# Performance work log

Hardware: AMD Instinct MI355X
Metric: run time of the kernel (lower is better)

The kernel has to match this reference:

```python
import jax, jax.numpy as jnp
import numpy as np

# pywt db3 analysis filters (dec_lo, dec_hi)
DB3_LO = np.array([0.035226291882100656, -0.08544127388224149, -0.13501102001039084,
                   0.4598775021193313, 0.8068915093133388, 0.3326705529509569], dtype=np.float32)
DB3_HI = np.array([-0.3326705529509569, 0.8068915093133388, -0.4598775021193313,
                   -0.13501102001039084, 0.08544127388224149, 0.035226291882100656], dtype=np.float32)
L_FILT = 6
J_LEVELS = 3
EPS = 1e-8


def _dwt_level(x):
    """One analysis level, zero-padding ('zero' mode, matches pywt/pytorch_wavelets).
    x: [B, N] -> (low [B, M], high [B, M]) with M = floor((N + L - 1) / 2).
    Uses true convolution (filters flipped) of the full zero-extended signal,
    downsampled at odd full-conv indices, implemented as one strided conv."""
    k = jnp.asarray(np.stack([DB3_LO[::-1], DB3_HI[::-1]])[:, None, :])  # [2,1,L]
    y = jax.lax.conv_general_dilated(x[:, None, :].astype(jnp.float32), k,
                                     window_strides=(2,),
                                     padding=[(L_FILT - 2, L_FILT - 1)])  # [B,2,M]
    return y[:, 0, :], y[:, 1, :]


def _dwt_stats(signals):
    """signals: [B, N]. Returns (mean of final low band, sum over levels of L2 norm
    of each high band) per row -- exactly what the torch loop computes per entity."""
    x = signals
    high_energy = jnp.zeros(signals.shape[0], signals.dtype)
    for _ in range(J_LEVELS):
        lo, hi = _dwt_level(x)
        high_energy = high_energy + jnp.sqrt(jnp.sum(hi * hi, axis=-1))
        x = lo
    return jnp.mean(x, axis=-1), high_energy


def _dirichlet_weight(key, low, high):
    a1 = jnp.clip(low, 1e-6)
    a2 = jnp.clip(high, 1e-6)
    s = a1 + a2
    a1, a2 = a1 / s, a2 / s
    # first component of Dirichlet([10*a1, 10*a2]) ~ Beta(10*a1, 10*a2)
    return jax.random.beta(key, 10.0 * a1, 10.0 * a2)


def setup_inputs() -> dict:
    key = jax.random.key(0)
    k1, k2, k3 = jax.random.split(key, 3)
    U, I, NNZ = 16384, 8192, 1000000
    user_idx = jax.random.randint(k1, (NNZ,), 0, U, dtype=jnp.int32)
    item_idx = jax.random.randint(k2, (NNZ,), 0, I, dtype=jnp.int32)
    values = jax.random.uniform(k3, (NNZ,), dtype=jnp.float32)
    return {"user_idx": user_idx, "item_idx": item_idx, "values": values,
            "num_users": U, "num_items": I}


def reference(user_idx, item_idx, values, num_users, num_items):
    # item popularity
    counts = jax.ops.segment_sum(jnp.ones_like(values), item_idx, num_segments=num_items)
    log_counts = jnp.log1p(counts)
    pop = jax.ops.segment_sum(values * log_counts[item_idx], item_idx, num_segments=num_items)
    pop = pop / (jnp.linalg.norm(pop) + EPS)
    # user activity
    act = jax.ops.segment_sum(values / jnp.log1p(pop[item_idx] + EPS),
                              user_idx, num_segments=num_users)
    act = act / (jnp.linalg.norm(act) + EPS)
    # batched dense signals + DWT (replaces per-entity python loop)
    Su = jnp.zeros((num_users, num_items), values.dtype).at[user_idx, item_idx].set(
        values * (1.0 + act[user_idx]))
    u_low, u_high = _dwt_stats(Su)
    Si = jnp.zeros((num_items, num_users), values.dtype).at[item_idx, user_idx].set(
        values * (1.0 + pop[item_idx]))
    i_low, i_high = _dwt_stats(Si)
    ku, ki = jax.random.split(jax.random.key(42))
    upw = _dirichlet_weight(ku, u_low, u_high)
    ipw = _dirichlet_weight(ki, i_low, i_high)
    return (upw, 1.0 - upw, ipw, 1.0 - ipw, act, pop)
```

## Files before the change

kernel.cpp:

```cpp
#include <hip/hip_runtime.h>
#include <stdint.h>

#define PARTITIONABLE 1

typedef unsigned long long ull;

#define NUM_U 16384
#define NUM_I 8192
#define CAP_U 160
#define CAP_I 256

#define OFF_UPW 0
#define OFF_UMW 16384
#define OFF_IPW 32768
#define OFF_IMW 40960
#define OFF_ACT 49152
#define OFF_POP 65536

struct K2 { uint32_t a, b; };

__host__ __device__ inline void tf2x32(uint32_t k0, uint32_t k1, uint32_t& x0, uint32_t& x1) {
  const uint32_t ks2 = k0 ^ k1 ^ 0x1BD11BDAu;
  x0 += k0; x1 += k1;
#define TF_R(r) { x0 += x1; x1 = (x1 << (r)) | (x1 >> (32 - (r))); x1 ^= x0; }
  TF_R(13) TF_R(15) TF_R(26) TF_R(6)
  x0 += k1; x1 += ks2 + 1u;
  TF_R(17) TF_R(29) TF_R(16) TF_R(24)
  x0 += ks2; x1 += k0 + 2u;
  TF_R(13) TF_R(15) TF_R(26) TF_R(6)
  x0 += k0; x1 += k1 + 3u;
  TF_R(17) TF_R(29) TF_R(16) TF_R(24)
  x0 += k1; x1 += ks2 + 4u;
  TF_R(13) TF_R(15) TF_R(26) TF_R(6)
  x0 += ks2; x1 += k0 + 5u;
#undef TF_R
}

__host__ __device__ inline K2 tf_enc(K2 k, uint32_t x0, uint32_t x1) {
  tf2x32(k.a, k.b, x0, x1);
  K2 r; r.a = x0; r.b = x1; return r;
}

__host__ __device__ inline void split2(K2 k, K2& c0, K2& c1) {
#if PARTITIONABLE
  c0 = tf_enc(k, 0u, 0u);
  c1 = tf_enc(k, 0u, 1u);
#else
  K2 p = tf_enc(k, 0u, 2u);
  K2 q = tf_enc(k, 1u, 3u);
  c0.a = p.a; c0.b = q.a;
  c1.a = p.b; c1.b = q.b;
#endif
}

__device__ inline void split3(K2 k, K2& c0, K2& c1, K2& c2) {
#if PARTITIONABLE
  c0 = tf_enc(k, 0u, 0u);
  c1 = tf_enc(k, 0u, 1u);
  c2 = tf_enc(k, 0u, 2u);
#else
  K2 p = tf_enc(k, 0u, 3u);
  K2 q = tf_enc(k, 1u, 4u);
  K2 r = tf_enc(k, 2u, 5u);
  c0.a = p.a; c0.b = q.a;
  c1.a = r.a; c1.b = p.b;
  c2.a = q.b; c2.b = r.b;
#endif
}

__device__ inline uint32_t draw_bits(K2 k) {
  K2 e = tf_enc(k, 0u, 0u);
#if PARTITIONABLE
  return e.a ^ e.b;
#else
  return e.a;
#endif
}

__device__ inline K2 elem_key(K2 k, uint32_t i, uint32_t B) {
#if PARTITIONABLE
  return tf_enc(k, 0u, i);
#else
  if (i < (B >> 1)) {
    K2 p = tf_enc(k, 2u * i, B + 2u * i);
    K2 q = tf_enc(k, 2u * i + 1u, B + 2u * i + 1u);
    K2 r; r.a = p.a; r.b = q.a; return r;
  } else {
    uint32_t j = 2u * i - B;
    K2 p = tf_enc(k, j, 2u * i);
    K2 q = tf_enc(k, j + 1u, 2u * i + 1u);
    K2 r; r.a = p.b; r.b = q.b; return r;
  }
#endif
}

__device__ inline float u01_bits(uint32_t b) {
  return __uint_as_float((b >> 9) | 0x3F800000u) - 1.0f;
}

__device__ inline float erfinv_f32(float x) {
  float w = -log1pf(-x * x);
  float p;
  if (w < 5.0f) {
    w = w - 2.5f;
    p = 2.81022636e-08f;
    p = fmaf(p, w, 3.43273939e-07f);
    p = fmaf(p, w, -3.5233877e-06f);
    p = fmaf(p, w, -4.39150654e-06f);
    p = fmaf(p, w, 0.00021858087f);
    p = fmaf(p, w, -0.00125372503f);
    p = fmaf(p, w, -0.00417768164f);
    p = fmaf(p, w, 0.246640727f);
    p = fmaf(p, w, 1.50140941f);
  } else {
    w = sqrtf(w) - 3.0f;
    p = -0.000200214257f;
    p = fmaf(p, w, 0.000100950558f);
    p = fmaf(p, w, 0.00134934322f);
    p = fmaf(p, w, -0.00367342844f);
    p = fmaf(p, w, 0.00573950773f);
    p = fmaf(p, w, -0.0076224613f);
    p = fmaf(p, w, 0.00943887047f);
    p = fmaf(p, w, 1.00167406f);
    p = fmaf(p, w, 2.83297682f);
  }
  return p * x;
}

__device__ float log_gamma_sample(K2 key, float alpha_orig) {
  const bool boost = (alpha_orig >= 1.0f);
  const float alpha = boost ? alpha_orig : (alpha_orig + 1.0f);
  const float d = alpha - 0.33333334f;
  const float c = 0.33333334f / sqrtf(d);

  K2 k0, sub;
  split2(key, k0, sub);
  const float u_boost = u01_bits(draw_bits(sub));

  K2 kcur = k0;
  float X = 0.0f, V = 1.0f, U = 2.0f;
  while ((U >= 1.0f - 0.0331f * (X * X)) &&
         (logf(U) >= X * 0.5f + d * ((1.0f - V) + logf(V)))) {
    K2 knext, xk, Uk;
    split3(kcur, knext, xk, Uk);
    kcur = knext;
    float x, v;
    K2 ik = xk;
    do {
      K2 in0, isub;
      split2(ik, in0, isub);
      ik = in0;
      float f = u01_bits(draw_bits(isub));
      float u = fmaxf(-0.99999994f, f * 2.0f + (-0.99999994f));
      x = 1.41421356f * erfinv_f32(u);
      v = 1.0f + x * c;
    } while (v <= 0.0f);
    X = x * x;
    V = (v * v) * v;
    U = u01_bits(draw_bits(Uk));
  }
  float lg = logf(d * V);
  if (!boost) lg += log1pf(-u_boost) / alpha_orig;
  return lg;
}


__global__ __launch_bounds__(256) void zero_kernel(ull* p, int n) {
  int i = blockIdx.x * 256 + threadIdx.x;
  if (i < n) p[i] = 0ull;
}

__global__ __launch_bounds__(256) void count_fill_kernel(
    const int* __restrict__ user, const int* __restrict__ item, int n,
    int* __restrict__ fu, int* __restrict__ fi,
    uint32_t* __restrict__ lu, uint32_t* __restrict__ li) {
  for (int k = blockIdx.x * 256 + threadIdx.x; k < n; k += gridDim.x * 256) {
    int it = item[k];
    int q = atomicAdd(&fi[it], 1);
    if (q < CAP_I) li[(size_t)it * CAP_I + q] = (uint32_t)k;
    int u = user[k];
    int p = atomicAdd(&fu[u], 1);
    if (p < CAP_U) lu[(size_t)u * CAP_U + p] = (uint32_t)k;
  }
}

__global__ __launch_bounds__(256) void pop_wave_kernel(
    const int* __restrict__ fi, const uint32_t* __restrict__ li,
    const float* __restrict__ values,
    float* __restrict__ pop, double* __restrict__ nrm2) {
  __shared__ float red[4];
  int lane = threadIdx.x & 63, wid = threadIdx.x >> 6;
  int i = blockIdx.x * 4 + wid;
  int cnt = fi[i];
  int cr = cnt < CAP_I ? cnt : CAP_I;
  long long s = 0;
  for (int e = lane; e < cr; e += 64)
    s += (long long)llrintf(values[li[(size_t)i * CAP_I + e]] * 4294967296.0f);
  for (int o = 32; o > 0; o >>= 1) s += __shfl_down(s, o);
  if (lane == 0) {
    float svf = (float)((double)(ull)s * (1.0 / 4294967296.0));
    float p = svf * log1pf((float)cnt);
    pop[i] = p;
    red[wid] = p * p;
  }
  __syncthreads();
  if (threadIdx.x == 0)
    atomicAdd(nrm2, (double)(red[0] + red[1] + red[2] + red[3]));
}

__global__ __launch_bounds__(256) void pop_norm_kernel(float* __restrict__ pop,
                                                       const double* __restrict__ nrm2,
                                                       float* __restrict__ out) {
  int i = blockIdx.x * 256 + threadIdx.x;
  if (i < NUM_I) {
    float nrm = sqrtf((float)(*nrm2));
    float v = pop[i] / (nrm + 1e-8f);
    pop[i] = v;
    out[OFF_POP + i] = v;
  }
}

__global__ __launch_bounds__(256) void act_wave_kernel(
    const int* __restrict__ fu, const uint32_t* __restrict__ lu,
    const int* __restrict__ item, const float* __restrict__ values,
    const float* __restrict__ pop,
    float* __restrict__ act, double* __restrict__ nrm2) {
  __shared__ float red[4];
  int lane = threadIdx.x & 63, wid = threadIdx.x >> 6;
  int u = blockIdx.x * 4 + wid;
  int cnt = fu[u];
  int cr = cnt < CAP_U ? cnt : CAP_U;
  long long s = 0;
  for (int e = lane; e < cr; e += 64) {
    uint32_t k = lu[(size_t)u * CAP_U + e];
    float term = values[k] / log1pf(pop[item[k]] + 1e-8f);
    s += (long long)llrintf(term * 16777216.0f);
  }
  for (int o = 32; o > 0; o >>= 1) s += __shfl_down(s, o);
  if (lane == 0) {
    float a = (float)((double)(ull)s * (1.0 / 16777216.0));
    act[u] = a;
    red[wid] = a * a;
  }
  __syncthreads();
  if (threadIdx.x == 0)
    atomicAdd(nrm2, (double)(red[0] + red[1] + red[2] + red[3]));
}

__global__ __launch_bounds__(256) void act_norm_kernel(float* __restrict__ act,
                                                       const double* __restrict__ nrm2,
                                                       float* __restrict__ out) {
  int u = blockIdx.x * 256 + threadIdx.x;
  if (u < NUM_U) {
    float nrm = sqrtf((float)(*nrm2));
    float v = act[u] / (nrm + 1e-8f);
    act[u] = v;
    out[OFF_ACT + u] = v;
  }
}

__device__ inline uint32_t evencomp(uint32_t x) {
  x = (x | (x >> 1)) & 0x55555555u;
  x = (x | (x >> 1)) & 0x33333333u;
  x = (x | (x >> 2)) & 0x0F0F0F0Fu;
  x = (x | (x >> 4)) & 0x00FF00FFu;
  x = (x | (x >> 8)) & 0x0000FFFFu;
  return x;
}
template <int NWIN>
__device__ inline uint32_t hword(const uint32_t* B, int i) {
  uint32_t a = (2 * i < NWIN) ? B[2 * i] : 0u;
  uint32_t b = (2 * i + 1 < NWIN) ? B[2 * i + 1] : 0u;
  return evencomp(a) | (evencomp(b) << 16);
}
template <int NWIN>
__device__ inline uint32_t tword(const uint32_t* B, int w) {
  uint32_t h = hword<NWIN>(B, w);
  uint32_t hp = (w > 0) ? hword<NWIN>(B, w - 1) : 0u;
  return h | (h << 1) | (h << 2) | (hp >> 31) | (hp >> 30);
}

template <int NWORDS>
__device__ inline int scan_bits(const uint32_t* __restrict__ W, uint16_t* __restrict__ P,
                                int tid, int* __restrict__ isc, int* __restrict__ tot) {
  constexpr int WPT = (NWORDS + 255) / 256;
  __syncthreads();
  uint32_t w[WPT];
  int v = 0;
#pragma unroll
  for (int j = 0; j < WPT; ++j) {
    int idx = tid * WPT + j;
    w[j] = (idx < NWORDS) ? W[idx] : 0u;
    v += __popc(w[j]);
  }
  int lane = tid & 63, wid = tid >> 6;
  int incl = v;
  for (int off = 1; off < 64; off <<= 1) {
    int y = __shfl_up(incl, off, 64);
    if (lane >= off) incl += y;
  }
  if (lane == 63) isc[wid] = incl;
  __syncthreads();
  int base = 0;
  for (int ww = 0; ww < wid; ++ww) base += isc[ww];
  int run = base + incl - v;
#pragma unroll
  for (int j = 0; j < WPT; ++j) {
    int idx = tid * WPT + j;
    if (idx < NWORDS) P[idx] = (uint16_t)run;
    run += __popc(w[j]);
  }
  if (tid == 255) *tot = run;
  __syncthreads();
  return *tot;
}

template <int NWORDS>
__device__ inline void build_wl(const uint32_t* __restrict__ T, const uint16_t* __restrict__ P,
                                uint16_t* __restrict__ wl, int tid) {
  for (int w = tid; w < NWORDS; w += 256) {
    uint32_t bits = T[w];
    int r0 = P[w], i = 0;
    while (bits) {
      int b = __ffs(bits) - 1; bits &= bits - 1u;
      wl[r0 + i] = (uint16_t)((w << 5) + b);
      ++i;
    }
  }
}

template <int NIN>
__device__ inline void gather6(const uint32_t* __restrict__ B, const uint16_t* __restrict__ P,
                               const float* __restrict__ V, int m,
                               float& lo_o, float& hi_o) {
  int c0 = 2 * m - 4; c0 = c0 < 0 ? 0 : c0;
  int c1 = 2 * m + 1; c1 = c1 > NIN - 1 ? NIN - 1 : c1;
  int w0 = c0 >> 5, w1 = c1 >> 5;
  uint32_t b0 = B[w0];
  uint32_t mlo = ~((1u << (c0 & 31)) - 1u);
  uint32_t mhi = (uint32_t)(((uint64_t)1u << ((c1 & 31) + 1)) - 1u);
  uint32_t sel0, sel1; uint32_t b1 = 0;
  if (w1 == w0) { sel0 = b0 & mlo & mhi; sel1 = 0u; }
  else { b1 = B[w1]; sel0 = b0 & mlo; sel1 = b1 & mhi; }
  float tv0 = 0.0f, tv1 = 0.0f, tv2 = 0.0f, tv3 = 0.0f, tv4 = 0.0f, tv5 = 0.0f;
  int tp1 = 2 * m + 1;
  uint32_t s = sel0;
  while (s) {
    int b = __ffs(s) - 1; s &= s - 1u;
    int c = (w0 << 5) + b;
    int idx = (int)P[w0] + __popc(b0 & ((1u << b) - 1u));
    float v = V[idx];
    int t = tp1 - c;
    if (t == 0) tv0 = v; else if (t == 1) tv1 = v; else if (t == 2) tv2 = v;
    else if (t == 3) tv3 = v; else if (t == 4) tv4 = v; else tv5 = v;
  }
  s = sel1;
  while (s) {
    int b = __ffs(s) - 1; s &= s - 1u;
    int c = (w1 << 5) + b;
    int idx = (int)P[w1] + __popc(b1 & ((1u << b) - 1u));
    float v = V[idx];
    int t = tp1 - c;
    if (t == 0) tv0 = v; else if (t == 1) tv1 = v; else if (t == 2) tv2 = v;
    else if (t == 3) tv3 = v; else if (t == 4) tv4 = v; else tv5 = v;
  }
  float lo = 0.0f, hi = 0.0f;
  lo += 0.035226291882100656f * tv0;  hi += -0.3326705529509569f * tv0;
  lo += -0.08544127388224149f * tv1;  hi += 0.8068915093133388f * tv1;
  lo += -0.13501102001039084f * tv2;  hi += -0.4598775021193313f * tv2;
  lo += 0.4598775021193313f * tv3;    hi += -0.13501102001039084f * tv3;
  lo += 0.8068915093133388f * tv4;    hi += 0.08544127388224149f * tv4;
  lo += 0.3326705529509569f * tv5;    hi += 0.035226291882100656f * tv5;
  lo_o = lo; hi_o = hi;
}

__device__ inline int rank_of(const uint32_t* __restrict__ B, const uint16_t* __restrict__ P,
                              int m) {
  int w = m >> 5;
  return (int)P[w] + __popc(B[w] & ((1u << (m & 31)) - 1u));
}

constexpr int align4c(int x) { return (x + 3) & ~3; }
constexpr int cmax(int a, int b) { return a > b ? a : b; }

constexpr int dwt_shm_bytes(int NCOLS, int M1, int M2, int M3, int CAP) {
  int NW = NCOLS / 32, NW1 = (M1 + 31) / 32, NW2 = (M2 + 31) / 32, NW3 = (M3 + 31) / 32;
  int SZ_RB = cmax(cmax(align4c(NW * 4 + NW * 2), align4c(NW2 * 4 + 4 * CAP * 2)),
                   align4c(5 * CAP * 2));
  int SZ_RC = cmax(align4c(NW1 * 4 + NW1 * 2), align4c(NW3 * 4 + NW3 * 2 + NW2 * 2));
  return (M1 + 12) * 4 + CAP * 4 + SZ_RB + SZ_RC + align4c(3 * CAP * 2) + 64;
}

template <int NCOLS, int M1, int M2, int M3, int CAP>
__global__ __launch_bounds__(256) void dwt_rows_kernel(
    const uint32_t* __restrict__ klist, const int* __restrict__ rowlen,
    const int* __restrict__ colsrc, const float* __restrict__ values,
    const float* __restrict__ scale_vec,
    float* __restrict__ low_out, float* __restrict__ high_out) {
  constexpr int NW = NCOLS / 32;
  constexpr int NW1 = (M1 + 31) / 32;
  constexpr int NW2 = (M2 + 31) / 32;
  constexpr int NW3 = (M3 + 31) / 32;
  constexpr uint32_t MK1 = (M1 & 31) ? ((1u << (M1 & 31)) - 1u) : 0xFFFFFFFFu;
  constexpr uint32_t MK2 = (M2 & 31) ? ((1u << (M2 & 31)) - 1u) : 0xFFFFFFFFu;
  constexpr uint32_t MK3 = (M3 & 31) ? ((1u << (M3 & 31)) - 1u) : 0xFFFFFFFFu;
  constexpr int SZ_RB = cmax(cmax(align4c(NW * 4 + NW * 2), align4c(NW2 * 4 + 4 * CAP * 2)),
                             align4c(5 * CAP * 2));
  constexpr int SZ_RC = cmax(align4c(NW1 * 4 + NW1 * 2), align4c(NW3 * 4 + NW3 * 2 + NW2 * 2));

  extern __shared__ char smroot[];
  float* buf = (float*)smroot;
  char* pA = smroot + (M1 + 12) * 4;
  int* slot = (int*)pA;
  float* sval = (float*)pA;
  char* pB = pA + CAP * 4;
  uint32_t* bitmap = (uint32_t*)pB;
  uint16_t* prefix = (uint16_t*)(pB + NW * 4);
  uint32_t* T2 = (uint32_t*)pB;
  uint16_t* wl2 = (uint16_t*)(pB + NW2 * 4);
  uint16_t* wl3 = (uint16_t*)pB;
  char* pC = pB + SZ_RB;
  uint32_t* T1 = (uint32_t*)pC;
  uint16_t* p1 = (uint16_t*)(pC + NW1 * 4);
  uint32_t* T3 = (uint32_t*)pC;
  uint16_t* p3 = (uint16_t*)(pC + NW3 * 4);
  uint16_t* p2 = (uint16_t*)(pC + NW3 * 4 + NW3 * 2);
  char* pD = pC + SZ_RC;
  uint16_t* wl1 = (uint16_t*)pD;
  char* pE = pD + align4c(3 * CAP * 2);
  int* isc = (int*)pE;
  int* tot = isc + 4;
  float* red = (float*)pE;

  const int r = blockIdx.x;
  const int tid = threadIdx.x;
  const float scale = 1.0f + scale_vec[r];
  int n = rowlen[r];
  if (n > CAP) n = CAP;
  const size_t krow = (size_t)r * CAP;

  {
    constexpr int NB4 = (M1 + 12) / 4;
    float4 z; z.x = 0.0f; z.y = 0.0f; z.z = 0.0f; z.w = 0.0f;
    for (int i = tid; i < NB4; i += 256) ((float4*)buf)[i] = z;
    for (int i = NB4 * 4 + tid; i < M1 + 12; i += 256) buf[i] = 0.0f;
  }
  for (int i = tid; i < NW; i += 256) bitmap[i] = 0u;
  for (int i = tid; i < CAP; i += 256) slot[i] = 0;
  __syncthreads();

  for (int e = tid; e < n; e += 256) {
    int c = colsrc[klist[krow + e]];
    atomicOr(&bitmap[c >> 5], 1u << (c & 31));
  }
  const int nw_cnt = scan_bits<NW>(bitmap, prefix, tid, isc, tot);

  for (int e = tid; e < n; e += 256) {
    uint32_t k = klist[krow + e];
    int c = colsrc[k];
    atomicMax(&slot[rank_of(bitmap, prefix, c)], (int)k + 1);
  }
  __syncthreads();

  for (int rr = tid; rr < nw_cnt; rr += 256)
    sval[rr] = values[slot[rr] - 1] * scale;
  for (int w = tid; w < NW1; w += 256) {
    uint32_t t = tword<NW>(bitmap, w);
    if (w == NW1 - 1) t &= MK1;
    T1[w] = t;
  }
  const int n1 = scan_bits<NW1>(T1, p1, tid, isc, tot);
  build_wl<NW1>(T1, p1, wl1, tid);
  __syncthreads();

  float h1 = 0.0f;
  for (int idx = tid; idx < n1; idx += 256) {
    int m = wl1[idx];
    float lo, hi;
    gather6<NCOLS>(bitmap, prefix, sval, m, lo, hi);
    buf[4 + m] = lo;
    h1 += hi * hi;
  }
  __syncthreads();

  for (int w = tid; w < NW2; w += 256) {
    uint32_t t = tword<NW1>(T1, w);
    if (w == NW2 - 1) t &= MK2;
    T2[w] = t;
  }
  const int n2 = scan_bits<NW2>(T2, p2, tid, isc, tot);
  build_wl<NW2>(T2, p2, wl2, tid);
  for (int w = tid; w < NW3; w += 256) {
    uint32_t t = tword<NW2>(T2, w);
    if (w == NW3 - 1) t &= MK3;
    T3[w] = t;
  }
  __syncthreads();

  float h2 = 0.0f;
  {
    int nb = (n2 + 255) >> 8;
    for (int b = 0; b < nb; ++b) {
      int idx = (b << 8) + tid;
      bool ok = idx < n2;
      int m = ok ? wl2[idx] : 0;
      const float* s = buf + 2 * m + 5;
      float x0 = s[0], x1 = s[-1], x2 = s[-2], x3 = s[-3], x4 = s[-4], x5 = s[-5];
      __syncthreads();
      if (ok) {
        float lo = 0.0f, hi = 0.0f;
        lo += 0.035226291882100656f * x0;  hi += -0.3326705529509569f * x0;
        lo += -0.08544127388224149f * x1;  hi += 0.8068915093133388f * x1;
        lo += -0.13501102001039084f * x2;  hi += -0.4598775021193313f * x2;
        lo += 0.4598775021193313f * x3;    hi += -0.13501102001039084f * x3;
        lo += 0.8068915093133388f * x4;    hi += 0.08544127388224149f * x4;
        lo += 0.3326705529509569f * x5;    hi += 0.035226291882100656f * x5;
        buf[4 + m] = lo;
        h2 += hi * hi;
      }
    }
  }
  __syncthreads();
  for (int idx = tid; idx < n1; idx += 256) {
    int m = wl1[idx];
    if (m < M2 && !((T2[m >> 5] >> (m & 31)) & 1u)) buf[4 + m] = 0.0f;
  }
  if (tid < 8) buf[4 + M2 + tid] = 0.0f;

  const int n3 = scan_bits<NW3>(T3, p3, tid, isc, tot);
  build_wl<NW3>(T3, p3, wl3, tid);
  __syncthreads();

  float h3 = 0.0f, slo = 0.0f;
  for (int idx = tid; idx < n3; idx += 256) {
    int m = wl3[idx];
    const float* s = buf + 2 * m + 5;
    float x0 = s[0], x1 = s[-1], x2 = s[-2], x3 = s[-3], x4 = s[-4], x5 = s[-5];
    float lo = 0.0f, hi = 0.0f;
    lo += 0.035226291882100656f * x0;  hi += -0.3326705529509569f * x0;
    lo += -0.08544127388224149f * x1;  hi += 0.8068915093133388f * x1;
    lo += -0.13501102001039084f * x2;  hi += -0.4598775021193313f * x2;
    lo += 0.4598775021193313f * x3;    hi += -0.13501102001039084f * x3;
    lo += 0.8068915093133388f * x4;    hi += 0.08544127388224149f * x4;
    lo += 0.3326705529509569f * x5;    hi += 0.035226291882100656f * x5;
    slo += lo;
    h3 += hi * hi;
  }

  for (int o = 32; o > 0; o >>= 1) {
    h1 += __shfl_down(h1, o);
    h2 += __shfl_down(h2, o);
    h3 += __shfl_down(h3, o);
    slo += __shfl_down(slo, o);
  }
  __syncthreads();
  int w = tid >> 6, lane = tid & 63;
  if (lane == 0) { red[w] = h1; red[4 + w] = h2; red[8 + w] = h3; red[12 + w] = slo; }
  __syncthreads();
  if (tid == 0) {
    float s1 = red[0] + red[1] + red[2] + red[3];
    float s2 = red[4] + red[5] + red[6] + red[7];
    float s3 = red[8] + red[9] + red[10] + red[11];
    float sl = red[12] + red[13] + red[14] + red[15];
    low_out[r] = sl / (float)M3;
    high_out[r] = sqrtf(s1) + sqrtf(s2) + sqrtf(s3);
  }
}

__global__ __launch_bounds__(256) void beta_kernel(
    const float* __restrict__ u_low, const float* __restrict__ u_high,
    const float* __restrict__ i_low, const float* __restrict__ i_high,
    float* __restrict__ out, K2 kAu, K2 kBu, K2 kAi, K2 kBi) {
  int t = blockIdx.x * 256 + threadIdx.x;
  if (t >= NUM_U + NUM_I) return;
  float low, high;
  K2 ka, kb;
  int o0, o1;
  if (t < NUM_U) {
    low = u_low[t]; high = u_high[t];
    ka = elem_key(kAu, (uint32_t)t, (uint32_t)NUM_U);
    kb = elem_key(kBu, (uint32_t)t, (uint32_t)NUM_U);
    o0 = OFF_UPW + t; o1 = OFF_UMW + t;
  } else {
    int j = t - NUM_U;
    low = i_low[j]; high = i_high[j];
    ka = elem_key(kAi, (uint32_t)j, (uint32_t)NUM_I);
    kb = elem_key(kBi, (uint32_t)j, (uint32_t)NUM_I);
    o0 = OFF_IPW + j; o1 = OFF_IMW + j;
  }
  float a1 = fmaxf(low, 1e-6f);
  float a2 = fmaxf(high, 1e-6f);
  float s = a1 + a2;
  a1 = a1 / s;
  a2 = a2 / s;
  float lga = log_gamma_sample(ka, 10.0f * a1);
  float lgb = log_gamma_sample(kb, 10.0f * a2);
  float m = fmaxf(lga, lgb);
  float na = expf(lga - m);
  float nb = expf(lgb - m);
  float w = na / (na + nb);
  out[o0] = w;
  out[o1] = 1.0f - w;
}

extern "C" void kernel_launch(void* const* d_in, const int* in_sizes, int n_in,
                              void* d_out, int out_size, void* d_ws, size_t ws_size,
                              hipStream_t stream) {
  const int* user_idx = (const int*)d_in[0];
  const int* item_idx = (const int*)d_in[1];
  const float* values = (const float*)d_in[2];
  const int NNZ = in_sizes[0];

  char* ws = (char*)d_ws;
  double* nrm2_pop = (double*)(ws + 0);
  double* nrm2_act = (double*)(ws + 8);
  float* pop = (float*)(ws + 229392);
  float* act = (float*)(ws + 262160);
  int* fill_u = (int*)(ws + 327696);
  int* fill_i = (int*)(ws + 393232);
  float* u_low = (float*)(ws + 426000);
  float* u_high = (float*)(ws + 491536);
  float* i_low = (float*)(ws + 557072);
  float* i_high = (float*)(ws + 589840);
  uint32_t* klist_u = (uint32_t*)(ws + 622608);
  uint32_t* klist_i = (uint32_t*)(ws + 11108368);
  float* out = (float*)d_out;

  K2 root; root.a = 0u; root.b = 42u;
  K2 ku, ki, kAu, kBu, kAi, kBi;
  split2(root, ku, ki);
  split2(ku, kAu, kBu);
  split2(ki, kAi, kBi);

  zero_kernel<<<1, 256, 0, stream>>>((ull*)ws, 2);
  zero_kernel<<<48, 256, 0, stream>>>((ull*)(ws + 327696), 98304 / 8);
  count_fill_kernel<<<1024, 256, 0, stream>>>(user_idx, item_idx, NNZ,
                                              fill_u, fill_i, klist_u, klist_i);
  pop_wave_kernel<<<NUM_I / 4, 256, 0, stream>>>(fill_i, klist_i, values, pop, nrm2_pop);
  pop_norm_kernel<<<NUM_I / 256, 256, 0, stream>>>(pop, nrm2_pop, out);
  act_wave_kernel<<<NUM_U / 4, 256, 0, stream>>>(fill_u, klist_u, item_idx, values,
                                                 pop, act, nrm2_act);
  act_norm_kernel<<<NUM_U / 256, 256, 0, stream>>>(act, nrm2_act, out);

  constexpr int U_SHM = dwt_shm_bytes(8192, 4098, 2051, 1028, CAP_U);
  constexpr int I_SHM = dwt_shm_bytes(16384, 8194, 4099, 2052, CAP_I);
  hipFuncSetAttribute((const void*)dwt_rows_kernel<8192, 4098, 2051, 1028, CAP_U>,
                      hipFuncAttributeMaxDynamicSharedMemorySize, U_SHM);
  hipFuncSetAttribute((const void*)dwt_rows_kernel<16384, 8194, 4099, 2052, CAP_I>,
                      hipFuncAttributeMaxDynamicSharedMemorySize, I_SHM);

  dwt_rows_kernel<8192, 4098, 2051, 1028, CAP_U><<<NUM_U, 256, U_SHM, stream>>>(
      klist_u, fill_u, item_idx, values, act, u_low, u_high);
  dwt_rows_kernel<16384, 8194, 4099, 2052, CAP_I><<<NUM_I, 256, I_SHM, stream>>>(
      klist_i, fill_i, user_idx, values, pop, i_low, i_high);

  beta_kernel<<<(NUM_U + NUM_I + 255) / 256, 256, 0, stream>>>(
      u_low, u_high, i_low, i_high, out, kAu, kBu, kAi, kBi);
}
```

Before: 407.5 us.

## Carry per-entry values in registers in DWT and split beta into gamma+combine

In the DWT row kernel, each thread now loads its single klist entry, column and scaled value once into registers. It reuses them for the bitmap insert, the rank computation and the final value write, instead of re-reading klist/colsrc and then gathering values through the slot indices. The beta sampler is split into a gamma kernel that gives each log-gamma sample its own thread in 64-wide blocks, plus a combine kernel. The split is meant to double parallelism and cut divergence in the rejection-sampling loops, at the cost of an extra launch and a workspace round trip. It relies on CAP being at most the block size, which a static assert enforces.

```diff
diff --git a/kernel.cpp b/kernel.cpp
--- a/kernel.cpp
+++ b/kernel.cpp
@@ -397,6 +397,7 @@
     const int* __restrict__ colsrc, const float* __restrict__ values,
     const float* __restrict__ scale_vec,
     float* __restrict__ low_out, float* __restrict__ high_out) {
+  static_assert(CAP <= 256, "register-carry staging requires CAP <= blockDim");
   constexpr int NW = NCOLS / 32;
   constexpr int NW1 = (M1 + 31) / 32;
   constexpr int NW2 = (M2 + 31) / 32;
@@ -437,7 +438,6 @@
   const float scale = 1.0f + scale_vec[r];
   int n = rowlen[r];
   if (n > CAP) n = CAP;
-  const size_t krow = (size_t)r * CAP;
 
   {
     constexpr int NB4 = (M1 + 12) / 4;
@@ -446,24 +446,27 @@
     for (int i = NB4 * 4 + tid; i < M1 + 12; i += 256) buf[i] = 0.0f;
   }
   for (int i = tid; i < NW; i += 256) bitmap[i] = 0u;
-  for (int i = tid; i < CAP; i += 256) slot[i] = 0;
-  __syncthreads();
-
-  for (int e = tid; e < n; e += 256) {
-    int c = colsrc[klist[krow + e]];
-    atomicOr(&bitmap[c >> 5], 1u << (c & 31));
-  }
-  const int nw_cnt = scan_bits<NW>(bitmap, prefix, tid, isc, tot);
-
-  for (int e = tid; e < n; e += 256) {
-    uint32_t k = klist[krow + e];
-    int c = colsrc[k];
-    atomicMax(&slot[rank_of(bitmap, prefix, c)], (int)k + 1);
-  }
-  __syncthreads();
-
-  for (int rr = tid; rr < nw_cnt; rr += 256)
-    sval[rr] = values[slot[rr] - 1] * scale;
+  if (tid < CAP) slot[tid] = 0;
+  __syncthreads();
+
+  const bool have = tid < n;
+  uint32_t my_k = 0; int my_c = 0; float my_v = 0.0f;
+  if (have) {
+    my_k = klist[(size_t)r * CAP + tid];
+    my_c = colsrc[my_k];
+    my_v = values[my_k] * scale;
+    atomicOr(&bitmap[my_c >> 5], 1u << (my_c & 31));
+  }
+  scan_bits<NW>(bitmap, prefix, tid, isc, tot);
+
+  int my_rank = 0;
+  if (have) {
+    my_rank = rank_of(bitmap, prefix, my_c);
+    atomicMax(&slot[my_rank], (int)my_k + 1);
+  }
+  __syncthreads();
+
+  if (have && slot[my_rank] == (int)my_k + 1) sval[my_rank] = my_v;
   for (int w = tid; w < NW1; w += 256) {
     uint32_t t = tword<NW>(bitmap, w);
     if (w == NW1 - 1) t &= MK1;
@@ -567,38 +570,46 @@
   }
 }
 
-__global__ __launch_bounds__(256) void beta_kernel(
+__global__ __launch_bounds__(64) void gamma_kernel(
     const float* __restrict__ u_low, const float* __restrict__ u_high,
     const float* __restrict__ i_low, const float* __restrict__ i_high,
-    float* __restrict__ out, K2 kAu, K2 kBu, K2 kAi, K2 kBi) {
-  int t = blockIdx.x * 256 + threadIdx.x;
-  if (t >= NUM_U + NUM_I) return;
+    float* __restrict__ lgbuf, K2 kAu, K2 kBu, K2 kAi, K2 kBi) {
+  const int TOT = NUM_U + NUM_I;
+  int t = blockIdx.x * 64 + threadIdx.x;
+  if (t >= 2 * TOT) return;
+  int ab = t >= TOT ? 1 : 0;
+  int ent = ab ? t - TOT : t;
   float low, high;
-  K2 ka, kb;
-  int o0, o1;
-  if (t < NUM_U) {
-    low = u_low[t]; high = u_high[t];
-    ka = elem_key(kAu, (uint32_t)t, (uint32_t)NUM_U);
-    kb = elem_key(kBu, (uint32_t)t, (uint32_t)NUM_U);
-    o0 = OFF_UPW + t; o1 = OFF_UMW + t;
+  K2 key;
+  if (ent < NUM_U) {
+    low = u_low[ent]; high = u_high[ent];
+    key = elem_key(ab ? kBu : kAu, (uint32_t)ent, (uint32_t)NUM_U);
   } else {
-    int j = t - NUM_U;
+    int j = ent - NUM_U;
     low = i_low[j]; high = i_high[j];
-    ka = elem_key(kAi, (uint32_t)j, (uint32_t)NUM_I);
-    kb = elem_key(kBi, (uint32_t)j, (uint32_t)NUM_I);
-    o0 = OFF_IPW + j; o1 = OFF_IMW + j;
+    key = elem_key(ab ? kBi : kAi, (uint32_t)j, (uint32_t)NUM_I);
   }
   float a1 = fmaxf(low, 1e-6f);
   float a2 = fmaxf(high, 1e-6f);
   float s = a1 + a2;
-  a1 = a1 / s;
-  a2 = a2 / s;
-  float lga = log_gamma_sample(ka, 10.0f * a1);
-  float lgb = log_gamma_sample(kb, 10.0f * a2);
+  float alpha = ab ? (10.0f * (a2 / s)) : (10.0f * (a1 / s));
+  lgbuf[t] = log_gamma_sample(key, alpha);
+}
+
+__global__ __launch_bounds__(256) void combine_kernel(
+    const float* __restrict__ lgbuf, float* __restrict__ out) {
+  const int TOT = NUM_U + NUM_I;
+  int t = blockIdx.x * 256 + threadIdx.x;
+  if (t >= TOT) return;
+  float lga = lgbuf[t];
+  float lgb = lgbuf[TOT + t];
   float m = fmaxf(lga, lgb);
   float na = expf(lga - m);
   float nb = expf(lgb - m);
   float w = na / (na + nb);
+  int o0, o1;
+  if (t < NUM_U) { o0 = OFF_UPW + t; o1 = OFF_UMW + t; }
+  else { int j = t - NUM_U; o0 = OFF_IPW + j; o1 = OFF_IMW + j; }
   out[o0] = w;
   out[o1] = 1.0f - w;
 }
@@ -614,6 +625,7 @@
   char* ws = (char*)d_ws;
   double* nrm2_pop = (double*)(ws + 0);
   double* nrm2_act = (double*)(ws + 8);
+  float* lgbuf = (float*)(ws + 16);
   float* pop = (float*)(ws + 229392);
   float* act = (float*)(ws + 262160);
   int* fill_u = (int*)(ws + 327696);
@@ -654,6 +666,8 @@
   dwt_rows_kernel<16384, 8194, 4099, 2052, CAP_I><<<NUM_I, 256, I_SHM, stream>>>(
       klist_i, fill_i, user_idx, values, pop, i_low, i_high);
 
-  beta_kernel<<<(NUM_U + NUM_I + 255) / 256, 256, 0, stream>>>(
-      u_low, u_high, i_low, i_high, out, kAu, kBu, kAi, kBi);
-}
+  const int TOT2 = 2 * (NUM_U + NUM_I);
+  gamma_kernel<<<(TOT2 + 63) / 64, 64, 0, stream>>>(
+      u_low, u_high, i_low, i_high, lgbuf, kAu, kBu, kAi, kBi);
+  combine_kernel<<<(NUM_U + NUM_I + 255) / 256, 256, 0, stream>>>(lgbuf, out);
+}
```

Result: no change. 400.6 us (-1.7%).
